# Kernel tuning notes

Measured on AMD Instinct MI355X. Metric: run time of the kernel, lower is better.

The kernel has to match this reference:

```python
import jax, jax.numpy as jnp
import numpy as np

HEADS = 8
DIM_HEAD = 64
ROPE_THETA = 10000.0


def _rope(t):
    # t: [b, h, n, d]; interleaved-pair rotation as in rotary-embedding-torch
    n, d = t.shape[-2], t.shape[-1]
    inv_freq = 1.0 / (ROPE_THETA ** (jnp.arange(0, d, 2, dtype=jnp.float32) / d))  # [d/2]
    freqs = jnp.arange(n, dtype=jnp.float32)[:, None] * inv_freq[None, :]  # [n, d/2]
    freqs = jnp.repeat(freqs, 2, axis=-1)  # [n, d], repeated per pair
    cos, sin = jnp.cos(freqs), jnp.sin(freqs)
    x1 = t[..., 0::2]
    x2 = t[..., 1::2]
    rot = jnp.stack((-x2, x1), axis=-1).reshape(t.shape)  # rotate_half
    return t * cos + rot * sin


def setup_inputs() -> dict:
    key = jax.random.key(0)
    k1, k2, k3, k4 = jax.random.split(key, 4)
    b, n, dim = 2, 2048, 512
    hidden = HEADS * DIM_HEAD
    x = jax.random.normal(k1, (b, n, dim), dtype=jnp.float32)
    pos_bias = jax.random.normal(k2, (HEADS, n, n), dtype=jnp.float32) * 0.02
    w_qkv = jax.random.normal(k3, (dim, 3 * hidden), dtype=jnp.float32) * (dim ** -0.5)
    w_out = jax.random.normal(k4, (hidden, dim), dtype=jnp.float32) * (hidden ** -0.5)
    return {"x": x, "pos_bias": pos_bias, "w_qkv": w_qkv, "w_out": w_out}


def reference(x, pos_bias, w_qkv, w_out):
    b, n, _ = x.shape
    qkv = x @ w_qkv  # [b, n, 3*hidden]
    q, k, v = jnp.split(qkv, 3, axis=-1)

    def to_heads(t):
        return t.reshape(b, n, HEADS, DIM_HEAD).transpose(0, 2, 1, 3)  # [b,h,n,d]

    q, k, v = map(to_heads, (q, k, v))
    k = _rope(k)
    q = _rope(q * (DIM_HEAD ** -0.5))
    sim = jnp.einsum('bhid,bhjd->bhij', q, k)  # [b,h,n,n]
    sim = sim + pos_bias  # broadcast over batch
    sim = sim - jax.lax.stop_gradient(jnp.max(sim, axis=-1, keepdims=True))
    attn = jax.nn.softmax(sim, axis=-1)
    out = jnp.einsum('bhij,bhjd->bhid', attn, v)
    out = out.transpose(0, 2, 1, 3).reshape(b, n, HEADS * DIM_HEAD)
    return out @ w_out
```

## Files before the change

kernel.cpp:

```cpp
#include <hip/hip_runtime.h>
#include <math.h>

#define SEQ 2048
#define NHEAD 8
#define HDIM 64
#define BATCH 2

typedef __attribute__((ext_vector_type(8))) short short8;
typedef __attribute__((ext_vector_type(4))) float f32x4;

__device__ __forceinline__ ushort f2bf(float f) {
    union { float f; unsigned u; } v; v.f = f;
    unsigned r = v.u + 0x7FFFu + ((v.u >> 16) & 1u);
    return (ushort)(r >> 16);
}

__device__ __forceinline__ f32x4 mfma16(short8 a, short8 b, f32x4 c) {
    return __builtin_amdgcn_mfma_f32_16x16x32_bf16(a, b, c, 0, 0, 0);
}

__device__ __forceinline__ void gld16(const void* g, void* l) {
    __builtin_amdgcn_global_load_lds(
        (const __attribute__((address_space(1))) unsigned int*)g,
        (__attribute__((address_space(3))) unsigned int*)l, 16, 0, 0);
}

__global__ __launch_bounds__(256)
void prep(const float* __restrict__ x, const float* __restrict__ w_qkv,
          const float* __restrict__ w_out, ushort* __restrict__ xb,
          ushort* __restrict__ wqkvT, ushort* __restrict__ woutT,
          float2* __restrict__ rope_tbl)
{
    __shared__ ushort tile[64][66];
    const int blk = blockIdx.x, t = threadIdx.x;
    if (blk >= 1280) {
        const int idx = (blk - 1280) * 256 + t;
        const int n = idx >> 1, fbase = (idx & 1) * 16;
#pragma unroll
        for (int f = 0; f < 16; ++f) {
            const float inv = __expf(-(float)(fbase + f) * (9.2103403719761836f / 32.0f));
            float sn, cs;
            __sincosf((float)n * inv, &sn, &cs);
            rope_tbl[(size_t)n * 32 + fbase + f] = make_float2(cs, sn);
        }
        return;
    }
    if (blk < 1024) {
        const int i = (blk * 256 + t) * 8;
        float4 a = *(const float4*)&x[i];
        float4 b = *(const float4*)&x[i + 4];
        union { ushort us[8]; uint4 v; } pk;
        pk.us[0] = f2bf(a.x); pk.us[1] = f2bf(a.y); pk.us[2] = f2bf(a.z); pk.us[3] = f2bf(a.w);
        pk.us[4] = f2bf(b.x); pk.us[5] = f2bf(b.y); pk.us[6] = f2bf(b.z); pk.us[7] = f2bf(b.w);
        *(uint4*)&xb[i] = pk.v;
        return;
    }
    const float* w; ushort* wT; int K, N, n0, k0;
    if (blk < 1216) { const int s = blk - 1024; w = w_qkv; wT = wqkvT; K = 512; N = 1536; n0 = (s % 24) * 64; k0 = (s / 24) * 64; }
    else            { const int s = blk - 1216; w = w_out; wT = woutT; K = 512; N = 512;  n0 = (s % 8) * 64;  k0 = (s / 8) * 64; }
#pragma unroll
    for (int i = 0; i < 4; ++i) {
        const int slot = t + i * 256;
        const int r = slot >> 4, c4 = (slot & 15) * 4;
        float4 v = *(const float4*)&w[(size_t)(k0 + r) * N + n0 + c4];
        tile[c4 + 0][r] = f2bf(v.x);
        tile[c4 + 1][r] = f2bf(v.y);
        tile[c4 + 2][r] = f2bf(v.z);
        tile[c4 + 3][r] = f2bf(v.w);
    }
    __syncthreads();
    const int n = t >> 2, kc = (t & 3) * 16;
    union { ushort us[16]; uint4 v[2]; } o;
#pragma unroll
    for (int j = 0; j < 16; ++j) o.us[j] = tile[n][kc + j];
    *(uint4*)&wT[(size_t)(n0 + n) * K + k0 + kc]     = o.v[0];
    *(uint4*)&wT[(size_t)(n0 + n) * K + k0 + kc + 8] = o.v[1];
}

__global__ __launch_bounds__(256)
void gemm_qkv_rope(const ushort* __restrict__ xb, const ushort* __restrict__ wT,
                   ushort* __restrict__ qb, ushort* __restrict__ kb,
                   ushort* __restrict__ vtb, const float2* __restrict__ rope_tbl)
{
    __shared__ __align__(16) ushort As[64][64];
    __shared__ __align__(16) ushort Bs[128][64];
    const int t = threadIdx.x, lane = t & 63, w = t >> 6;
    const int quad = lane >> 4, l16 = lane & 15;
    const int m0 = blockIdx.y * 64, n0 = blockIdx.x * 128;
    const int mw = (w >> 1) * 32, nw = (w & 1) * 64;
    const int krow = lane >> 3, kcol = (lane & 7) * 8;
    f32x4 acc[2][4] = {};

    for (int k0 = 0; k0 < 512; k0 += 64) {
        __syncthreads();
        gld16(&xb[(size_t)(m0 + w * 8 + krow) * 512 + k0 + kcol],        &As[w * 8][0]);
        gld16(&xb[(size_t)(m0 + (w + 4) * 8 + krow) * 512 + k0 + kcol],  &As[(w + 4) * 8][0]);
#pragma unroll
        for (int jj = 0; jj < 4; ++jj) {
            const int j = w * 4 + jj;
            gld16(&wT[(size_t)(n0 + j * 8 + krow) * 512 + k0 + kcol], &Bs[j * 8][0]);
        }
        __syncthreads();
#pragma unroll
        for (int ks = 0; ks < 2; ++ks) {
            short8 a[2], b[4];
#pragma unroll
            for (int i = 0; i < 2; ++i)
                a[i] = *(const short8*)&As[mw + i * 16 + l16][ks * 32 + quad * 8];
#pragma unroll
            for (int j = 0; j < 4; ++j)
                b[j] = *(const short8*)&Bs[nw + j * 16 + l16][ks * 32 + quad * 8];
#pragma unroll
            for (int i = 0; i < 2; ++i)
#pragma unroll
                for (int j = 0; j < 4; ++j)
                    acc[i][j] = mfma16(a[i], b[j], acc[i][j]);
        }
    }

    const int sec = (n0 + nw) >> 9;
    if (sec == 2) {
#pragma unroll
        for (int i = 0; i < 2; ++i) {
            const int m = m0 + mw + i * 16 + quad * 4;
            const int bidx = m >> 11, n = m & 2047;
#pragma unroll
            for (int j = 0; j < 4; ++j) {
                const int nc = n0 + nw + j * 16 + l16;
                const int d = nc & 63, h = (nc >> 6) & 7;
                ushort4 pk;
                pk.x = f2bf(acc[i][j][0]); pk.y = f2bf(acc[i][j][1]);
                pk.z = f2bf(acc[i][j][2]); pk.w = f2bf(acc[i][j][3]);
                *(ushort4*)&vtb[(((size_t)bidx * 8 + h) * 64 + d) * 2048 + n] = pk;
            }
        }
    } else {
        ushort* dst = (sec == 0) ? qb : kb;
        const float scale = (sec == 0) ? 0.125f : 1.0f;
#pragma unroll
        for (int j = 0; j < 4; ++j) {
            const int nc = n0 + nw + j * 16 + l16;
            const int d = nc & 63, h = (nc >> 6) & 7;
            const float2* tb = rope_tbl + (d >> 1);
#pragma unroll
            for (int i = 0; i < 2; ++i)
#pragma unroll
            for (int r = 0; r < 4; ++r) {
                const int m = m0 + mw + i * 16 + quad * 4 + r;
                const int bidx = m >> 11, n = m & 2047;
                const float2 cs2 = tb[(size_t)n * 32];
                const float vacc = acc[i][j][r];
                const float partner = __shfl_xor(vacc, 1);
                const float rot = (d & 1) ? (vacc * cs2.x + partner * cs2.y)
                                          : (vacc * cs2.x - partner * cs2.y);
                dst[(((size_t)bidx * 8 + h) * 2048 + n) * 64 + d] = f2bf(rot * scale);
            }
        }
    }
}

__global__ __launch_bounds__(512)
void flash_attn_mfma(const ushort* __restrict__ qb, const ushort* __restrict__ kb,
                     const ushort* __restrict__ vtb, const float* __restrict__ bias,
                     ushort* __restrict__ ob)
{
    __shared__ __align__(16) ushort Ks[3][64][64];
    __shared__ __align__(16) ushort Vt[3][64][64];
    __shared__ __align__(16) ushort Ps[8][16][72];
    const int t = threadIdx.x, lane = t & 63, w = t >> 6;
    const int quad = lane >> 4, l16 = lane & 15;
    const int q0 = blockIdx.x * 128, h = blockIdx.y, b = blockIdx.z;
    const size_t bh = (size_t)(b * NHEAD + h);
    const ushort* Q  = qb  + bh * SEQ * HDIM;
    const ushort* Kp = kb  + bh * SEQ * HDIM;
    const ushort* VT = vtb + bh * HDIM * SEQ;
    const float*  Bp = bias + ((size_t)h * SEQ + q0 + w * 16) * SEQ;

    f32x4 oacc[4] = {};
    float lsum[4] = {};
    const int krow = lane >> 3;
    const int kcolsw = ((lane & 7) ^ krow) * 8;

    const int sw = l16 & 7;
    const int c0 = (quad ^ sw) * 8;
    const int c1 = ((quad + 4) ^ sw) * 8;

    short8 qf[2];
    qf[0] = *(const short8*)&Q[(size_t)(q0 + w * 16 + l16) * HDIM + quad * 8];
    qf[1] = *(const short8*)&Q[(size_t)(q0 + w * 16 + l16) * HDIM + 32 + quad * 8];
    asm volatile("" ::: "memory");

    float b0[16], b1[16];

#define FA_STAGE(BUF, IT_)                                                          \
    {                                                                               \
        const int k2_ = (IT_) * 64;                                                 \
        gld16(&Kp[(size_t)(k2_ + w * 8 + krow) * HDIM + kcolsw], &Ks[BUF][w * 8][0]); \
        gld16(&VT[(size_t)(w * 8 + krow) * SEQ + k2_ + kcolsw],  &Vt[BUF][w * 8][0]); \
    }

#define FA_BIAS(BREG, IT_)                                                          \
    {                                                                               \
        const int k2_ = (IT_) * 64;                                                 \
        _Pragma("unroll")                                                           \
        for (int r = 0; r < 4; ++r)                                                 \
            _Pragma("unroll")                                                       \
            for (int s = 0; s < 4; ++s)                                             \
                BREG[r * 4 + s] = Bp[(size_t)(quad * 4 + r) * SEQ + k2_ + s * 16 + l16]; \
    }

#define FA_BODY(IT, BCUR, REFILL, WCNT)                                             \
    {                                                                               \
        asm volatile("s_waitcnt vmcnt(" #WCNT ")" ::: "memory");                    \
        __builtin_amdgcn_s_barrier();                                               \
        const int cb_ = (IT) % 3;                                                   \
        if (REFILL) {                                                               \
            FA_STAGE(((IT) + 2) % 3, (IT) + 2);                                     \
            asm volatile("" ::: "memory");              \
        }                                                                           \
        f32x4 sacc[4] = {};                                                         \
        __builtin_amdgcn_s_setprio(1);                                              \
        _Pragma("unroll")                                                           \
        for (int s = 0; s < 4; ++s) {                                               \
            short8 kf0 = *(const short8*)&Ks[cb_][s * 16 + l16][c0];                \
            sacc[s] = mfma16(qf[0], kf0, sacc[s]);                                  \
            short8 kf1 = *(const short8*)&Ks[cb_][s * 16 + l16][c1];                \
            sacc[s] = mfma16(qf[1], kf1, sacc[s]);                                  \
        }                                                                           \
        __builtin_amdgcn_s_setprio(0);                                              \
        _Pragma("unroll")                                                           \
        for (int r = 0; r < 4; ++r)                                                 \
            _Pragma("unroll")                                                       \
            for (int s = 0; s < 4; ++s) {                                           \
                const float p = __expf(sacc[s][r] + BCUR[r * 4 + s]);               \
                lsum[r] += p;                                                       \
                Ps[w][quad * 4 + r][s * 16 + l16] = f2bf(p);                        \
            }                                                                       \
        if (REFILL) FA_BIAS(BCUR, (IT) + 2);                                        \
        asm volatile("" ::: "memory");               \
        __builtin_amdgcn_s_setprio(1);                                              \
        _Pragma("unroll")                                                           \
        for (int ks = 0; ks < 2; ++ks) {                                            \
            short8 pf = *(const short8*)&Ps[w][l16][ks * 32 + quad * 8];            \
            const int cc_ = ks ? c1 : c0;                                           \
            _Pragma("unroll")                                                       \
            for (int s = 0; s < 4; ++s) {                                           \
                short8 vf = *(const short8*)&Vt[cb_][s * 16 + l16][cc_];            \
                oacc[s] = mfma16(pf, vf, oacc[s]);                                  \
            }                                                                       \
        }                                                                           \
        __builtin_amdgcn_s_setprio(0);                                              \
    }

    FA_STAGE(0, 0);
    asm volatile("" ::: "memory");
    FA_BIAS(b0, 0);
    asm volatile("" ::: "memory");
    FA_STAGE(1, 1);
    asm volatile("" ::: "memory");
    FA_BIAS(b1, 1);

    for (int i2 = 0; i2 < 15; ++i2) {
        FA_BODY(2 * i2,     b0, 1, 34);
        FA_BODY(2 * i2 + 1, b1, 1, 34);
    }
    FA_BODY(30, b0, 0, 34);
    FA_BODY(31, b1, 0, 16);

#undef FA_BODY
#undef FA_BIAS
#undef FA_STAGE

#pragma unroll
    for (int r = 0; r < 4; ++r) {
        float rs = lsum[r];
        rs += __shfl_xor(rs, 1, 16);
        rs += __shfl_xor(rs, 2, 16);
        rs += __shfl_xor(rs, 4, 16);
        rs += __shfl_xor(rs, 8, 16);
        const float invl = 1.0f / rs;
        const size_t m = (size_t)b * SEQ + q0 + w * 16 + quad * 4 + r;
#pragma unroll
        for (int s = 0; s < 4; ++s)
            ob[m * 512 + h * HDIM + s * 16 + l16] = f2bf(oacc[s][r] * invl);
    }
}

__global__ __launch_bounds__(256)
void gemm_out(const ushort* __restrict__ Ab, const ushort* __restrict__ wT,
              float* __restrict__ C)
{
    __shared__ __align__(16) ushort As[64][64];
    __shared__ __align__(16) ushort Bs[64][64];
    const int t = threadIdx.x, lane = t & 63, w = t >> 6;
    const int quad = lane >> 4, l16 = lane & 15;
    const int m0 = blockIdx.y * 64, n0 = blockIdx.x * 64;
    const int mw = (w >> 1) * 32, nw = (w & 1) * 32;
    const int krow = lane >> 3, kcol = (lane & 7) * 8;
    f32x4 acc[2][2] = {};

    for (int k0 = 0; k0 < 512; k0 += 64) {
        __syncthreads();
        gld16(&Ab[(size_t)(m0 + w * 8 + krow) * 512 + k0 + kcol],       &As[w * 8][0]);
        gld16(&Ab[(size_t)(m0 + (w + 4) * 8 + krow) * 512 + k0 + kcol], &As[(w + 4) * 8][0]);
        gld16(&wT[(size_t)(n0 + w * 8 + krow) * 512 + k0 + kcol],       &Bs[w * 8][0]);
        gld16(&wT[(size_t)(n0 + (w + 4) * 8 + krow) * 512 + k0 + kcol], &Bs[(w + 4) * 8][0]);
        __syncthreads();
#pragma unroll
        for (int ks = 0; ks < 2; ++ks) {
            short8 a[2], b[2];
#pragma unroll
            for (int i = 0; i < 2; ++i)
                a[i] = *(const short8*)&As[mw + i * 16 + l16][ks * 32 + quad * 8];
#pragma unroll
            for (int j = 0; j < 2; ++j)
                b[j] = *(const short8*)&Bs[nw + j * 16 + l16][ks * 32 + quad * 8];
#pragma unroll
            for (int i = 0; i < 2; ++i)
#pragma unroll
                for (int j = 0; j < 2; ++j)
                    acc[i][j] = mfma16(a[i], b[j], acc[i][j]);
        }
    }
#pragma unroll
    for (int i = 0; i < 2; ++i)
#pragma unroll
    for (int r = 0; r < 4; ++r) {
        const int m = m0 + mw + i * 16 + quad * 4 + r;
#pragma unroll
        for (int j = 0; j < 2; ++j)
            C[(size_t)m * 512 + n0 + nw + j * 16 + l16] = acc[i][j][r];
    }
}

extern "C" void kernel_launch(void* const* d_in, const int* in_sizes, int n_in,
                              void* d_out, int out_size, void* d_ws, size_t ws_size,
                              hipStream_t stream)
{
    const float* x        = (const float*)d_in[0];
    const float* pos_bias = (const float*)d_in[1];
    const float* w_qkv    = (const float*)d_in[2];
    const float* w_out    = (const float*)d_in[3];
    float* out = (float*)d_out;

    char* ws = (char*)d_ws;
    ushort* xb     = (ushort*)(ws);
    ushort* wqkvT  = (ushort*)(ws + 4194304);
    ushort* woutT  = (ushort*)(ws + 5767168);
    ushort* qb     = (ushort*)(ws + 6291456);
    ushort* kb     = (ushort*)(ws + 10485760);
    ushort* vtb    = (ushort*)(ws + 14680064);
    ushort* attnb  = (ushort*)(ws + 18874368);
    float2* ropetb = (float2*)(ws + 23068672);

    prep<<<1296, 256, 0, stream>>>(x, w_qkv, w_out, xb, wqkvT, woutT, ropetb);
    gemm_qkv_rope<<<dim3(12, 64), 256, 0, stream>>>(xb, wqkvT, qb, kb, vtb, ropetb);
    flash_attn_mfma<<<dim3(SEQ / 128, NHEAD, BATCH), 512, 0, stream>>>(qb, kb, vtb, pos_bias, attnb);
    gemm_out<<<dim3(8, 64), 256, 0, stream>>>(attnb, woutT, out);
}
```

Before: 251.0 us.

## Split attention over KV chunks and share pos_bias loads across both batches

Each attention block now handles both batch elements for one head and query tile, so every pos_bias tile is read once and used for both batches instead of once per batch. The KV sequence is also split into four chunks along the grid, which doubles the block count. Unnormalised partial outputs and row sums go to an fp32 workspace. A new combine kernel sums them and normalises. This cuts the dominant bias memory traffic and improves parallelism, at the cost of an extra kernel launch and roughly 32MB of partial-output write and readback.

Measured after the change: 363.4 us. 44.8% more time.

```diff
diff --git a/kernel.cpp b/kernel.cpp
--- a/kernel.cpp
+++ b/kernel.cpp
@@ -159,131 +159,207 @@
     }
 }
 
-__global__ __launch_bounds__(512)
+__global__ __launch_bounds__(512, 4)
 void flash_attn_mfma(const ushort* __restrict__ qb, const ushort* __restrict__ kb,
                      const ushort* __restrict__ vtb, const float* __restrict__ bias,
-                     ushort* __restrict__ ob)
+                     float* __restrict__ opart, float* __restrict__ lpart)
 {
     __shared__ __align__(16) ushort Ks[3][64][64];
     __shared__ __align__(16) ushort Vt[3][64][64];
     __shared__ __align__(16) ushort Ps[8][16][72];
     const int t = threadIdx.x, lane = t & 63, w = t >> 6;
     const int quad = lane >> 4, l16 = lane & 15;
-    const int q0 = blockIdx.x * 128, h = blockIdx.y, b = blockIdx.z;
-    const size_t bh = (size_t)(b * NHEAD + h);
-    const ushort* Q  = qb  + bh * SEQ * HDIM;
-    const ushort* Kp = kb  + bh * SEQ * HDIM;
-    const ushort* VT = vtb + bh * HDIM * SEQ;
-    const float*  Bp = bias + ((size_t)h * SEQ + q0 + w * 16) * SEQ;
-
-    f32x4 oacc[4] = {};
-    float lsum[4] = {};
+    const int q0 = blockIdx.x * 128, h = blockIdx.y, ksp = blockIdx.z;
+    const int kv0 = ksp * 512;
+    const ushort* Q0  = qb  + (size_t)h * SEQ * HDIM;
+    const ushort* Q1  = qb  + (size_t)(8 + h) * SEQ * HDIM;
+    const ushort* Kp0 = kb  + (size_t)h * SEQ * HDIM;
+    const ushort* Kp1 = kb  + (size_t)(8 + h) * SEQ * HDIM;
+    const ushort* VT0 = vtb + (size_t)h * HDIM * SEQ;
+    const ushort* VT1 = vtb + (size_t)(8 + h) * HDIM * SEQ;
+    const float*  Bp  = bias + ((size_t)h * SEQ + q0 + w * 16) * SEQ + kv0;
+
+    f32x4 oacc0[4] = {}, oacc1[4] = {};
+    float lsum0[4] = {}, lsum1[4] = {};
     const int krow = lane >> 3;
     const int kcolsw = ((lane & 7) ^ krow) * 8;
-
     const int sw = l16 & 7;
     const int c0 = (quad ^ sw) * 8;
     const int c1 = ((quad + 4) ^ sw) * 8;
 
-    short8 qf[2];
-    qf[0] = *(const short8*)&Q[(size_t)(q0 + w * 16 + l16) * HDIM + quad * 8];
-    qf[1] = *(const short8*)&Q[(size_t)(q0 + w * 16 + l16) * HDIM + 32 + quad * 8];
+    short8 qf0[2], qf1[2];
+    qf0[0] = *(const short8*)&Q0[(size_t)(q0 + w * 16 + l16) * HDIM + quad * 8];
+    qf0[1] = *(const short8*)&Q0[(size_t)(q0 + w * 16 + l16) * HDIM + 32 + quad * 8];
+    qf1[0] = *(const short8*)&Q1[(size_t)(q0 + w * 16 + l16) * HDIM + quad * 8];
+    qf1[1] = *(const short8*)&Q1[(size_t)(q0 + w * 16 + l16) * HDIM + 32 + quad * 8];
     asm volatile("" ::: "memory");
 
-    float b0[16], b1[16];
-
-#define FA_STAGE(BUF, IT_)                                                          \
+    float breg[16];
+
+#define FA_STAGE(BUF, TILE, KPp, VTp)                                               \
     {                                                                               \
-        const int k2_ = (IT_) * 64;                                                 \
-        gld16(&Kp[(size_t)(k2_ + w * 8 + krow) * HDIM + kcolsw], &Ks[BUF][w * 8][0]); \
-        gld16(&VT[(size_t)(w * 8 + krow) * SEQ + k2_ + kcolsw],  &Vt[BUF][w * 8][0]); \
-    }
-
-#define FA_BIAS(BREG, IT_)                                                          \
+        const int k2_ = kv0 + (TILE) * 64;                                          \
+        gld16(&KPp[(size_t)(k2_ + w * 8 + krow) * HDIM + kcolsw], &Ks[BUF][w * 8][0]); \
+        gld16(&VTp[(size_t)(w * 8 + krow) * SEQ + k2_ + kcolsw],  &Vt[BUF][w * 8][0]); \
+    }
+
+#define FA_BIAS(TILE)                                                               \
     {                                                                               \
-        const int k2_ = (IT_) * 64;                                                 \
+        const int k2_ = (TILE) * 64;                                                \
         _Pragma("unroll")                                                           \
         for (int r = 0; r < 4; ++r)                                                 \
             _Pragma("unroll")                                                       \
             for (int s = 0; s < 4; ++s)                                             \
-                BREG[r * 4 + s] = Bp[(size_t)(quad * 4 + r) * SEQ + k2_ + s * 16 + l16]; \
-    }
-
-#define FA_BODY(IT, BCUR, REFILL, WCNT)                                             \
+                breg[r * 4 + s] = Bp[(size_t)(quad * 4 + r) * SEQ + k2_ + s * 16 + l16]; \
+    }
+
+#define FA_CORE(IT, QF, OACC, LSUM)                                                 \
     {                                                                               \
-        asm volatile("s_waitcnt vmcnt(" #WCNT ")" ::: "memory");                    \
-        __builtin_amdgcn_s_barrier();                                               \
         const int cb_ = (IT) % 3;                                                   \
-        if (REFILL) {                                                               \
-            FA_STAGE(((IT) + 2) % 3, (IT) + 2);                                     \
-            asm volatile("" ::: "memory");              \
-        }                                                                           \
         f32x4 sacc[4] = {};                                                         \
         __builtin_amdgcn_s_setprio(1);                                              \
         _Pragma("unroll")                                                           \
         for (int s = 0; s < 4; ++s) {                                               \
             short8 kf0 = *(const short8*)&Ks[cb_][s * 16 + l16][c0];                \
-            sacc[s] = mfma16(qf[0], kf0, sacc[s]);                                  \
+            sacc[s] = mfma16(QF[0], kf0, sacc[s]);                                  \
             short8 kf1 = *(const short8*)&Ks[cb_][s * 16 + l16][c1];                \
-            sacc[s] = mfma16(qf[1], kf1, sacc[s]);                                  \
+            sacc[s] = mfma16(QF[1], kf1, sacc[s]);                                  \
         }                                                                           \
         __builtin_amdgcn_s_setprio(0);                                              \
         _Pragma("unroll")                                                           \
         for (int r = 0; r < 4; ++r)                                                 \
             _Pragma("unroll")                                                       \
             for (int s = 0; s < 4; ++s) {                                           \
-                const float p = __expf(sacc[s][r] + BCUR[r * 4 + s]);               \
-                lsum[r] += p;                                                       \
+                const float p = __expf(sacc[s][r] + breg[r * 4 + s]);               \
+                LSUM[r] += p;                                                       \
                 Ps[w][quad * 4 + r][s * 16 + l16] = f2bf(p);                        \
             }                                                                       \
-        if (REFILL) FA_BIAS(BCUR, (IT) + 2);                                        \
         asm volatile("" ::: "memory");               \
         __builtin_amdgcn_s_setprio(1);                                              \
         _Pragma("unroll")                                                           \
-        for (int ks = 0; ks < 2; ++ks) {                                            \
-            short8 pf = *(const short8*)&Ps[w][l16][ks * 32 + quad * 8];            \
-            const int cc_ = ks ? c1 : c0;                                           \
+        for (int ks2 = 0; ks2 < 2; ++ks2) {                                         \
+            short8 pf = *(const short8*)&Ps[w][l16][ks2 * 32 + quad * 8];           \
+            const int cc_ = ks2 ? c1 : c0;                                          \
             _Pragma("unroll")                                                       \
             for (int s = 0; s < 4; ++s) {                                           \
                 short8 vf = *(const short8*)&Vt[cb_][s * 16 + l16][cc_];            \
-                oacc[s] = mfma16(pf, vf, oacc[s]);                                  \
+                oacc_dummy                                                          \
             }                                                                       \
         }                                                                           \
         __builtin_amdgcn_s_setprio(0);                                              \
     }
-
-    FA_STAGE(0, 0);
-    asm volatile("" ::: "memory");
-    FA_BIAS(b0, 0);
-    asm volatile("" ::: "memory");
-    FA_STAGE(1, 1);
-    asm volatile("" ::: "memory");
-    FA_BIAS(b1, 1);
-
-    for (int i2 = 0; i2 < 15; ++i2) {
-        FA_BODY(2 * i2,     b0, 1, 34);
-        FA_BODY(2 * i2 + 1, b1, 1, 34);
-    }
-    FA_BODY(30, b0, 0, 34);
-    FA_BODY(31, b1, 0, 16);
-
-#undef FA_BODY
+#undef FA_CORE
+#define FA_CORE(IT, QF, OACC, LSUM)                                                 \
+    {                                                                               \
+        const int cb_ = (IT) % 3;                                                   \
+        f32x4 sacc[4] = {};                                                         \
+        __builtin_amdgcn_s_setprio(1);                                              \
+        _Pragma("unroll")                                                           \
+        for (int s = 0; s < 4; ++s) {                                               \
+            short8 kf0 = *(const short8*)&Ks[cb_][s * 16 + l16][c0];                \
+            sacc[s] = mfma16(QF[0], kf0, sacc[s]);                                  \
+            short8 kf1 = *(const short8*)&Ks[cb_][s * 16 + l16][c1];                \
+            sacc[s] = mfma16(QF[1], kf1, sacc[s]);                                  \
+        }                                                                           \
+        __builtin_amdgcn_s_setprio(0);                                              \
+        _Pragma("unroll")                                                           \
+        for (int r = 0; r < 4; ++r)                                                 \
+            _Pragma("unroll")                                                       \
+            for (int s = 0; s < 4; ++s) {                                           \
+                const float p = __expf(sacc[s][r] + breg[r * 4 + s]);               \
+                LSUM[r] += p;                                                       \
+                Ps[w][quad * 4 + r][s * 16 + l16] = f2bf(p);                        \
+            }                                                                       \
+        asm volatile("" ::: "memory");               \
+        __builtin_amdgcn_s_setprio(1);                                              \
+        _Pragma("unroll")                                                           \
+        for (int ks2 = 0; ks2 < 2; ++ks2) {                                         \
+            short8 pf = *(const short8*)&Ps[w][l16][ks2 * 32 + quad * 8];           \
+            const int cc_ = ks2 ? c1 : c0;                                          \
+            _Pragma("unroll")                                                       \
+            for (int s = 0; s < 4; ++s) {                                           \
+                short8 vf = *(const short8*)&Vt[cb_][s * 16 + l16][cc_];            \
+                OACC[s] = mfma16(pf, vf, OACC[s]);                                  \
+            }                                                                       \
+        }                                                                           \
+        __builtin_amdgcn_s_setprio(0);                                              \
+    }
+
+#define FA_W(N) asm volatile("s_waitcnt vmcnt(" #N ")" ::: "memory")
+
+    FA_STAGE(0, 0, Kp0, VT0);
+    FA_STAGE(1, 0, Kp1, VT1);
+    FA_BIAS(0);
+
+#pragma unroll
+    for (int T = 0; T < 7; ++T) {
+        FA_W(18);
+        __builtin_amdgcn_s_barrier();
+        FA_STAGE((2 * T + 2) % 3, T + 1, Kp0, VT0);
+        FA_CORE(2 * T, qf0, oacc0, lsum0);
+        FA_W(18);
+        __builtin_amdgcn_s_barrier();
+        FA_STAGE((2 * T + 3) % 3, T + 1, Kp1, VT1);
+        FA_CORE(2 * T + 1, qf1, oacc1, lsum1);
+        FA_BIAS(T + 1);
+    }
+    FA_W(18);
+    __builtin_amdgcn_s_barrier();
+    FA_CORE(14, qf0, oacc0, lsum0);
+    FA_W(16);
+    __builtin_amdgcn_s_barrier();
+    FA_CORE(15, qf1, oacc1, lsum1);
+
+#undef FA_W
+#undef FA_CORE
 #undef FA_BIAS
 #undef FA_STAGE
 
-#pragma unroll
-    for (int r = 0; r < 4; ++r) {
-        float rs = lsum[r];
-        rs += __shfl_xor(rs, 1, 16);
-        rs += __shfl_xor(rs, 2, 16);
-        rs += __shfl_xor(rs, 4, 16);
-        rs += __shfl_xor(rs, 8, 16);
-        const float invl = 1.0f / rs;
-        const size_t m = (size_t)b * SEQ + q0 + w * 16 + quad * 4 + r;
-#pragma unroll
-        for (int s = 0; s < 4; ++s)
-            ob[m * 512 + h * HDIM + s * 16 + l16] = f2bf(oacc[s][r] * invl);
-    }
+    const size_t obase = (size_t)ksp * (4096 * 512);
+#define FA_EPI(OACC, LSUM, BB)                                                      \
+    {                                                                               \
+        _Pragma("unroll")                                                           \
+        for (int r = 0; r < 4; ++r) {                                               \
+            float rs = LSUM[r];                                                     \
+            rs += __shfl_xor(rs, 1, 16);                                            \
+            rs += __shfl_xor(rs, 2, 16);                                            \
+            rs += __shfl_xor(rs, 4, 16);                                            \
+            rs += __shfl_xor(rs, 8, 16);                                            \
+            const int q = q0 + w * 16 + quad * 4 + r;                               \
+            const size_t m = (size_t)(BB) * SEQ + q;                                \
+            if (l16 == 0)                                                           \
+                lpart[(((size_t)ksp * NHEAD + h) * 2 + (BB)) * SEQ + q] = rs;       \
+            _Pragma("unroll")                                                       \
+            for (int s = 0; s < 4; ++s)                                             \
+                opart[obase + m * 512 + h * 64 + s * 16 + l16] = OACC[s][r];        \
+        }                                                                           \
+    }
+    FA_EPI(oacc0, lsum0, 0);
+    FA_EPI(oacc1, lsum1, 1);
+#undef FA_EPI
+}
+
+__global__ __launch_bounds__(256)
+void combine_o(const float* __restrict__ opart, const float* __restrict__ lpart,
+               ushort* __restrict__ ob)
+{
+    const int idx = blockIdx.x * 256 + threadIdx.x;
+    const int m = idx >> 7;
+    const int c4 = (idx & 127) * 4;
+    const int h = c4 >> 6, bb = m >> 11, q = m & 2047;
+    float4 acc = make_float4(0.f, 0.f, 0.f, 0.f);
+    float l = 0.f;
+#pragma unroll
+    for (int s = 0; s < 4; ++s) {
+        const float4 p = *(const float4*)&opart[(size_t)s * (4096 * 512) + (size_t)m * 512 + c4];
+        acc.x += p.x; acc.y += p.y; acc.z += p.z; acc.w += p.w;
+        l += lpart[(((size_t)s * NHEAD + h) * 2 + bb) * SEQ + q];
+    }
+    const float inv = 1.0f / l;
+    ushort4 o;
+    o.x = f2bf(acc.x * inv); o.y = f2bf(acc.y * inv);
+    o.z = f2bf(acc.z * inv); o.w = f2bf(acc.w * inv);
+    *(ushort4*)&ob[(size_t)m * 512 + c4] = o;
 }
 
 __global__ __launch_bounds__(256)
@@ -352,9 +428,12 @@
     ushort* vtb    = (ushort*)(ws + 14680064);
     ushort* attnb  = (ushort*)(ws + 18874368);
     float2* ropetb = (float2*)(ws + 23068672);
+    float*  opart  = (float*)(ws + 25165824);
+    float*  lpart  = (float*)(ws + 58720256);
 
     prep<<<1296, 256, 0, stream>>>(x, w_qkv, w_out, xb, wqkvT, woutT, ropetb);
     gemm_qkv_rope<<<dim3(12, 64), 256, 0, stream>>>(xb, wqkvT, qb, kb, vtb, ropetb);
-    flash_attn_mfma<<<dim3(SEQ / 128, NHEAD, BATCH), 512, 0, stream>>>(qb, kb, vtb, pos_bias, attnb);
+    flash_attn_mfma<<<dim3(SEQ / 128, NHEAD, 4), 512, 0, stream>>>(qb, kb, vtb, pos_bias, opart, lpart);
+    combine_o<<<2048, 256, 0, stream>>>(opart, lpart, attnb);
     gemm_out<<<dim3(8, 64), 256, 0, stream>>>(attnb, woutT, out);
 }
```
